# Performance work log

Hardware: AMD Instinct MI355X
Metric: run time of the kernel (lower is better)

The kernel has to match this reference:

```python
import jax, jax.numpy as jnp
import numpy as np

T, N = 256, 4000
DM, DI, H, DH = 178, 46, 64, 64  # macro dim, individual dim, lstm hidden, dense hidden
F = DI + H


def setup_inputs() -> dict:
    key = jax.random.key(0)
    ks = jax.random.split(key, 14)
    inp = {
        'macro_features': jax.random.normal(ks[0], (1, T, DM), jnp.float32),
        'individual_features': jax.random.normal(ks[1], (1, T, N, DI), jnp.float32),
        'masks': jax.random.randint(ks[2], (1, T, N, 1), 0, 2).astype(bool),
        'returns_tensor': 0.05 * jax.random.normal(ks[3], (1, T, N, 1), jnp.float32),
        # LSTM params (torch gate order: i, f, g, o)
        'W_ih': jax.random.normal(ks[4], (4 * H, DM), jnp.float32) / np.sqrt(DM).astype(np.float32),
        'W_hh': jax.random.normal(ks[5], (4 * H, H), jnp.float32) / np.sqrt(H).astype(np.float32),
        'b_ih': jnp.zeros((4 * H,), jnp.float32),
        'b_hh': jnp.zeros((4 * H,), jnp.float32),
        # Dense net: F -> DH -> DH -> 1, relu hidden, linear output
        'W1': jax.random.normal(ks[6], (DH, F), jnp.float32) / np.sqrt(F).astype(np.float32),
        'b1': jnp.zeros((DH,), jnp.float32),
        'W2': jax.random.normal(ks[7], (DH, DH), jnp.float32) / np.sqrt(DH).astype(np.float32),
        'b2': jnp.zeros((DH,), jnp.float32),
        'W3': jax.random.normal(ks[8], (1, DH), jnp.float32) / np.sqrt(DH).astype(np.float32),
        'b3': jnp.zeros((1,), jnp.float32),
    }
    return inp


def _lstm(x, W_ih, W_hh, b_ih, b_hh):
    # x: [T, DM] -> h_seq: [T, H]
    h0 = jnp.zeros((H,), x.dtype)
    c0 = jnp.zeros((H,), x.dtype)
    xz = x @ W_ih.T + (b_ih + b_hh)  # precompute input projection [T, 4H]

    def step(carry, zt):
        h, c = carry
        z = zt + h @ W_hh.T
        i, f, g, o = jnp.split(z, 4)
        i, f, o = jax.nn.sigmoid(i), jax.nn.sigmoid(f), jax.nn.sigmoid(o)
        g = jnp.tanh(g)
        c = f * c + i * g
        h = o * jnp.tanh(c)
        return (h, c), h

    _, h_seq = jax.lax.scan(step, (h0, c0), xz)
    return h_seq


def reference(macro_features, individual_features, masks, returns_tensor,
              W_ih, W_hh, b_ih, b_hh, W1, b1, W2, b2, W3, b3):
    # recurrent processing of macro features (batch = 1)
    h = _lstm(macro_features[0], W_ih, W_hh, b_ih, b_hh)  # [T, H]
    # tile macro state across assets and concat with individual features
    macro_tiled = jnp.broadcast_to(h[None, :, None, :], (1, T, N, H))
    dense_in = jnp.concatenate([individual_features, macro_tiled], axis=-1)  # [1,T,N,F]
    # pointwise MLP -> SDF weight per (t, asset)
    a = jax.nn.relu(jnp.einsum('btnf,hf->btnh', dense_in, W1) + b1)
    a = jax.nn.relu(jnp.einsum('btnh,gh->btng', a, W2) + b2)
    weights = jnp.einsum('btng,og->btno', a, W3) + b3  # [1,T,N,1]
    maskf = masks.astype(weights.dtype)
    weights = weights * maskf  # weights at valid positions (dense layout)
    weighted_returns = returns_tensor * weights  # already zero where masked out
    # ragged per-timestep segment sum == masked sum over assets
    sum_per_time = jnp.sum(weighted_returns, axis=(0, 2, 3))[:, None]  # [T,1]
    num_val_per_time = jnp.sum(maskf, axis=(0, 2, 3))  # [T]
    mean_num_val = jnp.mean(num_val_per_time)
    sum_per_time = sum_per_time / num_val_per_time[:, None] * mean_num_val  # normalize_w
    sdf = sum_per_time + 1.0
    return sdf, weights
```

## Files before the change

kernel.cpp:

```cpp
#include <hip/hip_runtime.h>
#include <hip/hip_bf16.h>
#include <math.h>

#define T 256
#define N 4000
#define DM 178
#define DI 46
#define H 64
#define DH 64
#define F (DI + DH)
#define GC 16
#define CN 250

typedef __attribute__((ext_vector_type(8))) short bf16x8;
typedef __attribute__((ext_vector_type(4))) float f32x4;

__device__ inline unsigned int f2bf(float f) {
  __hip_bfloat16 h = __float2bfloat16(f);
  unsigned short u;
  __builtin_memcpy(&u, &h, 2);
  return (unsigned int)u;
}

__device__ inline bf16x8 frag_read(const unsigned int* buf, int row, int kbyte) {
  const int b = (row << 7) + (kbyte ^ ((row & 7) << 4));
  return *reinterpret_cast<const bf16x8*>(reinterpret_cast<const char*>(buf) + b);
}
__device__ inline void sw_write32(unsigned int* buf, int row, int kbyte, unsigned int v) {
  const int b = (row << 7) + (kbyte ^ ((row & 7) << 4));
  buf[b >> 2] = v;
}
__device__ inline void sw_write16(unsigned int* buf, int row, int kbyte, unsigned short v) {
  const int b = (row << 7) + (kbyte ^ ((row & 7) << 4));
  *reinterpret_cast<unsigned short*>(reinterpret_cast<char*>(buf) + b) = v;
}

__device__ inline float frcp(float x) { return __builtin_amdgcn_rcpf(x); }
__device__ inline float fsig(float z) { return frcp(1.f + __expf(-z)); }
__device__ inline float ftanh(float x) {
  const float ax = fabsf(x);
  const float e = __expf(-2.f * ax);
  const float r = (1.f - e) * frcp(1.f + e);
  return copysignf(r, x);
}

__global__ __launch_bounds__(256) void k_xz(const float* __restrict__ x,
    const float* __restrict__ W_ih, const float* __restrict__ b_ih,
    const float* __restrict__ b_hh, float* __restrict__ xz) {
  const int t = blockIdx.x, j = threadIdx.x;
  __shared__ float xs[DM];
  if (j < DM) xs[j] = x[t * DM + j];
  __syncthreads();
  float acc = b_ih[j] + b_hh[j];
  const float* w = W_ih + j * DM;
  #pragma unroll 2
  for (int k = 0; k < DM; ++k) acc += w[k] * xs[k];
  xz[t * (4 * H) + j] = acc;
}

__global__ __launch_bounds__(256) void k_lstm(const float* __restrict__ xz,
    const float* __restrict__ W_hh, float* __restrict__ h_seq) {
  const int tid = threadIdx.x;
  __shared__ float4 hs4[16];
  __shared__ float zs[256];
  float* hs = reinterpret_cast<float*>(hs4);
  float4 wv4[16];
  const float4* wsrc = reinterpret_cast<const float4*>(W_hh + tid * 64);
  #pragma unroll
  for (int k = 0; k < 16; ++k) wv4[k] = wsrc[k];
  float c = 0.f;
  if (tid < H) hs[tid] = 0.f;
  float znext = xz[tid];
  __syncthreads();
  for (int t = 0; t < T; ++t) {
    const float zcur = znext;
    if (t + 1 < T) znext = xz[(t + 1) * 256 + tid];
    float a0 = 0.f, a1 = 0.f, a2 = 0.f, a3 = 0.f;
    #pragma unroll
    for (int k = 0; k < 16; ++k) {
      const float4 hv = hs4[k];
      a0 += wv4[k].x * hv.x; a1 += wv4[k].y * hv.y;
      a2 += wv4[k].z * hv.z; a3 += wv4[k].w * hv.w;
    }
    zs[tid] = zcur + ((a0 + a1) + (a2 + a3));
    __syncthreads();
    if (tid < H) {
      const float zi = zs[tid], zf = zs[H + tid], zg = zs[2 * H + tid], zo = zs[3 * H + tid];
      const float ig = fsig(zi), fg = fsig(zf), og = fsig(zo);
      const float gg = ftanh(zg);
      c = fg * c + ig * gg;
      const float h = og * ftanh(c);
      hs[tid] = h;
      h_seq[t * H + tid] = h;
    }
    __syncthreads();
  }
}

__global__ __launch_bounds__(64) void k_m1(const float* __restrict__ h_seq,
    const float* __restrict__ W1, const float* __restrict__ b1,
    float* __restrict__ m1g) {
  const int t = blockIdx.x, j = threadIdx.x;
  __shared__ float hsm[H];
  hsm[j] = h_seq[t * H + j];
  __syncthreads();
  float acc = b1[j];
  const float* w = W1 + j * F + DI;
  #pragma unroll
  for (int k = 0; k < H; ++k) acc += w[k] * hsm[k];
  m1g[t * DH + j] = acc;
}

__global__ __launch_bounds__(256) void k_mlp(
    const float* __restrict__ ind, const int* __restrict__ mask,
    const float* __restrict__ ret,
    const float* __restrict__ W1, const float* __restrict__ W2,
    const float* __restrict__ b2, const float* __restrict__ W3,
    const float* __restrict__ b3, const float* __restrict__ m1g,
    float* __restrict__ wout, float* __restrict__ p_wr, float* __restrict__ p_ct) {
  const int t = blockIdx.y, chunk = blockIdx.x, tid = threadIdx.x;
  const int lr = tid & 15;
  const int lq = (tid >> 4) & 3;
  const int wv = tid >> 6;

  __shared__ unsigned int XB[8192];
  __shared__ unsigned int WB1[2048];
  __shared__ unsigned int WB2[2048];
  __shared__ float m1s[DH], b2s[DH], w3s[DH];
  __shared__ float ws_sum[256];
  __shared__ float red[8];

  #pragma unroll
  for (int i = 0; i < 32; ++i) XB[tid + 256 * i] = 0u;
  #pragma unroll
  for (int i = 0; i < 8; ++i) WB1[tid + 256 * i] = 0u;
  __syncthreads();

  const size_t pos0 = (size_t)t * N + (size_t)chunk * CN;
  const float* xbase = ind + pos0 * DI;
  for (int i = tid; i < CN * DI / 2; i += 256) {
    const float2 v = *reinterpret_cast<const float2*>(xbase + 2 * i);
    const int row = i / 23, kp = i - row * 23;
    sw_write32(XB, row, kp * 4, f2bf(v.x) | (f2bf(v.y) << 16));
  }
  for (int i = tid; i < 64 * 23; i += 256) {
    const int n = i / 23, kp = i - n * 23;
    const float2 v = *reinterpret_cast<const float2*>(W1 + n * F + 2 * kp);
    sw_write32(WB1, n, kp * 4, f2bf(v.x) | (f2bf(v.y) << 16));
  }
  for (int i = tid; i < 64 * 32; i += 256) {
    const int n = i >> 5, kp = i & 31;
    const float2 v = *reinterpret_cast<const float2*>(W2 + n * DH + 2 * kp);
    sw_write32(WB2, n, kp * 4, f2bf(v.x) | (f2bf(v.y) << 16));
  }
  if (tid < DH) { m1s[tid] = m1g[t * DH + tid]; b2s[tid] = b2[tid]; w3s[tid] = W3[tid]; }
  __syncthreads();

  bf16x8 b1f[4][2];
  #pragma unroll
  for (int nt = 0; nt < 4; ++nt)
    #pragma unroll
    for (int ks = 0; ks < 2; ++ks)
      b1f[nt][ks] = frag_read(WB1, nt * 16 + lr, ks * 64 + lq * 16);

  const int rbase = wv * 64;
  #pragma unroll
  for (int mt = 0; mt < 4; ++mt) {
    const int arow = rbase + mt * 16 + lr;
    const bf16x8 a0 = frag_read(XB, arow, lq * 16);
    const bf16x8 a1 = frag_read(XB, arow, 64 + lq * 16);
    #pragma unroll
    for (int nt = 0; nt < 4; ++nt) {
      f32x4 acc = {0.f, 0.f, 0.f, 0.f};
      acc = __builtin_amdgcn_mfma_f32_16x16x32_bf16(a0, b1f[nt][0], acc, 0, 0, 0);
      acc = __builtin_amdgcn_mfma_f32_16x16x32_bf16(a1, b1f[nt][1], acc, 0, 0, 0);
      const int col = nt * 16 + lr;
      const float mv = m1s[col];
      #pragma unroll
      for (int r = 0; r < 4; ++r) {
        const float v = fmaxf(acc[r] + mv, 0.f);
        sw_write16(XB, rbase + mt * 16 + lq * 4 + r, col * 2, (unsigned short)f2bf(v));
      }
    }
  }

  bf16x8 b2f[4][2];
  #pragma unroll
  for (int nt = 0; nt < 4; ++nt)
    #pragma unroll
    for (int ks = 0; ks < 2; ++ks)
      b2f[nt][ks] = frag_read(WB2, nt * 16 + lr, ks * 64 + lq * 16);
  const float b3v = b3[0];

  #pragma unroll
  for (int mt = 0; mt < 4; ++mt) {
    const int arow = rbase + mt * 16 + lr;
    const bf16x8 a0 = frag_read(XB, arow, lq * 16);
    const bf16x8 a1 = frag_read(XB, arow, 64 + lq * 16);
    float s0 = 0.f, s1 = 0.f, s2 = 0.f, s3 = 0.f;
    #pragma unroll
    for (int nt = 0; nt < 4; ++nt) {
      f32x4 acc = {0.f, 0.f, 0.f, 0.f};
      acc = __builtin_amdgcn_mfma_f32_16x16x32_bf16(a0, b2f[nt][0], acc, 0, 0, 0);
      acc = __builtin_amdgcn_mfma_f32_16x16x32_bf16(a1, b2f[nt][1], acc, 0, 0, 0);
      const int col = nt * 16 + lr;
      const float bb = b2s[col], w3 = w3s[col];
      s0 += w3 * fmaxf(acc[0] + bb, 0.f);
      s1 += w3 * fmaxf(acc[1] + bb, 0.f);
      s2 += w3 * fmaxf(acc[2] + bb, 0.f);
      s3 += w3 * fmaxf(acc[3] + bb, 0.f);
    }
    #pragma unroll
    for (int off = 1; off < 16; off <<= 1) {
      s0 += __shfl_xor(s0, off);
      s1 += __shfl_xor(s1, off);
      s2 += __shfl_xor(s2, off);
      s3 += __shfl_xor(s3, off);
    }
    if (lr < 4) {
      const float v = (lr == 0) ? s0 : (lr == 1) ? s1 : (lr == 2) ? s2 : s3;
      ws_sum[rbase + mt * 16 + lq * 4 + lr] = v + b3v;
    }
  }
  __syncthreads();

  float wr_val = 0.f, ct_val = 0.f;
  if (tid < CN) {
    const size_t pos = pos0 + tid;
    const float mf = (mask[pos] != 0) ? 1.f : 0.f;
    const float wgt = ws_sum[tid] * mf;
    wout[pos] = wgt;
    wr_val = ret[pos] * wgt;
    ct_val = mf;
  }
  #pragma unroll
  for (int off = 32; off > 0; off >>= 1) {
    wr_val += __shfl_down(wr_val, off);
    ct_val += __shfl_down(ct_val, off);
  }
  if ((tid & 63) == 0) { red[wv] = wr_val; red[4 + wv] = ct_val; }
  __syncthreads();
  if (tid == 0) {
    p_wr[t * GC + chunk] = red[0] + red[1] + red[2] + red[3];
    p_ct[t * GC + chunk] = red[4] + red[5] + red[6] + red[7];
  }
}

__global__ __launch_bounds__(256) void k_fin(const float* __restrict__ p_wr,
    const float* __restrict__ p_ct, float* __restrict__ out) {
  const int t = threadIdx.x;
  float s = 0.f, c = 0.f;
  #pragma unroll
  for (int k = 0; k < GC; ++k) { s += p_wr[t * GC + k]; c += p_ct[t * GC + k]; }
  __shared__ float cs[T];
  cs[t] = c;
  for (int off = 128; off > 0; off >>= 1) {
    __syncthreads();
    if (t < off) cs[t] += cs[t + off];
  }
  __syncthreads();
  const float meanc = cs[0] * (1.0f / (float)T);
  out[t] = s / c * meanc + 1.0f;
}

extern "C" void kernel_launch(void* const* d_in, const int* in_sizes, int n_in,
                              void* d_out, int out_size, void* d_ws, size_t ws_size,
                              hipStream_t stream) {
  const float* macro = (const float*)d_in[0];
  const float* ind   = (const float*)d_in[1];
  const int*   mask  = (const int*)d_in[2];
  const float* ret   = (const float*)d_in[3];
  const float* W_ih  = (const float*)d_in[4];
  const float* W_hh  = (const float*)d_in[5];
  const float* b_ih  = (const float*)d_in[6];
  const float* b_hh  = (const float*)d_in[7];
  const float* W1    = (const float*)d_in[8];
  const float* b1    = (const float*)d_in[9];
  const float* W2    = (const float*)d_in[10];
  const float* b2    = (const float*)d_in[11];
  const float* W3    = (const float*)d_in[12];
  const float* b3    = (const float*)d_in[13];

  float* out = (float*)d_out;
  float* ws  = (float*)d_ws;
  float* xz    = ws;
  float* h_seq = xz + T * 4 * H;
  float* m1g   = h_seq + T * H;
  float* p_wr  = m1g + T * DH;
  float* p_ct  = p_wr + T * GC;

  k_xz  <<<dim3(T), dim3(256), 0, stream>>>(macro, W_ih, b_ih, b_hh, xz);
  k_lstm<<<dim3(1), dim3(256), 0, stream>>>(xz, W_hh, h_seq);
  k_m1  <<<dim3(T), dim3(64), 0, stream>>>(h_seq, W1, b1, m1g);
  k_mlp <<<dim3(GC, T), dim3(256), 0, stream>>>(ind, mask, ret, W1, W2, b2, W3, b3,
                                                m1g, out + T, p_wr, p_ct);
  k_fin <<<dim3(1), dim3(T), 0, stream>>>(p_wr, p_ct, out);
}
```

Baseline: 542.3 us.

## Cut LSTM step to one barrier via per-wave redundant cell update

```diff
diff --git a/kernel.cpp b/kernel.cpp
--- a/kernel.cpp
+++ b/kernel.cpp
@@ -61,39 +61,43 @@
 __global__ __launch_bounds__(256) void k_lstm(const float* __restrict__ xz,
     const float* __restrict__ W_hh, float* __restrict__ h_seq) {
   const int tid = threadIdx.x;
-  __shared__ float4 hs4[16];
-  __shared__ float zs[256];
-  float* hs = reinterpret_cast<float*>(hs4);
+  const int wv = tid >> 6;
+  const int j  = tid & 63;
+  __shared__ float4 hsw[4][16];
+  __shared__ float acts[2][256];
+
   float4 wv4[16];
-  const float4* wsrc = reinterpret_cast<const float4*>(W_hh + tid * 64);
+  const float4* wsrc = reinterpret_cast<const float4*>(W_hh + tid * H);
   #pragma unroll
   for (int k = 0; k < 16; ++k) wv4[k] = wsrc[k];
+
   float c = 0.f;
-  if (tid < H) hs[tid] = 0.f;
+  if (j < 16) hsw[wv][j] = make_float4(0.f, 0.f, 0.f, 0.f);
   float znext = xz[tid];
   __syncthreads();
+
   for (int t = 0; t < T; ++t) {
     const float zcur = znext;
     if (t + 1 < T) znext = xz[(t + 1) * 256 + tid];
     float a0 = 0.f, a1 = 0.f, a2 = 0.f, a3 = 0.f;
     #pragma unroll
     for (int k = 0; k < 16; ++k) {
-      const float4 hv = hs4[k];
+      const float4 hv = hsw[wv][k];
       a0 += wv4[k].x * hv.x; a1 += wv4[k].y * hv.y;
       a2 += wv4[k].z * hv.z; a3 += wv4[k].w * hv.w;
     }
-    zs[tid] = zcur + ((a0 + a1) + (a2 + a3));
+    const float z = zcur + ((a0 + a1) + (a2 + a3));
+    const float act = (wv == 2) ? ftanh(z) : fsig(z);
+    acts[t & 1][tid] = act;
     __syncthreads();
-    if (tid < H) {
-      const float zi = zs[tid], zf = zs[H + tid], zg = zs[2 * H + tid], zo = zs[3 * H + tid];
-      const float ig = fsig(zi), fg = fsig(zf), og = fsig(zo);
-      const float gg = ftanh(zg);
-      c = fg * c + ig * gg;
-      const float h = og * ftanh(c);
-      hs[tid] = h;
-      h_seq[t * H + tid] = h;
-    }
-    __syncthreads();
+    const float gi = acts[t & 1][j];
+    const float gf = acts[t & 1][H + j];
+    const float gg = acts[t & 1][2 * H + j];
+    const float go = acts[t & 1][3 * H + j];
+    c = gf * c + gi * gg;
+    const float h = go * ftanh(c);
+    reinterpret_cast<float*>(&hsw[wv][0])[j] = h;
+    if (wv == 0) h_seq[t * H + j] = h;
   }
 }
 
```

After: 528.7 us. -2.5%, faster.
